# Kernel optimization log

Hardware: AMD Instinct MI355X
Metric: run time of the kernel (lower is better)

The kernel has to match this reference:

```python
import jax, jax.numpy as jnp
import numpy as np

B, S, HID = 1, 2048, 2048
H, KV, D = 32, 8, 64          # num_heads, num_kv_heads, head_dim
N_REP = H // KV               # GQA groups = 4
FF = 8192
EPS = 1e-5
ROPE_THETA = 10000.0


def _rope_tables(seq_len, dim, dtype=jnp.float32):
    inv_freq = 1.0 / (ROPE_THETA ** (jnp.arange(0, dim, 2, dtype=jnp.float32) / dim))
    t = jnp.arange(seq_len, dtype=jnp.float32)
    freqs = jnp.outer(t, inv_freq)                 # [S, D/2]
    emb = jnp.concatenate([freqs, freqs], axis=-1) # [S, D]
    return jnp.cos(emb).astype(dtype)[None], jnp.sin(emb).astype(dtype)[None]  # [1,S,D]


def setup_inputs() -> dict:
    key = jax.random.key(0)
    ks = jax.random.split(key, 10)
    s = 0.02
    cos, sin = _rope_tables(S, D)
    return {
        "hidden_states": jax.random.normal(ks[0], (B, S, HID), jnp.float32),
        "cos": cos, "sin": sin,
        "wq": jax.random.normal(ks[1], (HID, H * D), jnp.float32) * s,
        "wk": jax.random.normal(ks[2], (HID, KV * D), jnp.float32) * s,
        "wv": jax.random.normal(ks[3], (HID, KV * D), jnp.float32) * s,
        "wo": jax.random.normal(ks[4], (H * D, HID), jnp.float32) * s,
        "w_ln1": jnp.ones((HID,), jnp.float32),
        "w_ln2": jnp.ones((HID,), jnp.float32),
        "w_gate": jax.random.normal(ks[5], (HID, FF), jnp.float32) * s,
        "w_up": jax.random.normal(ks[6], (HID, FF), jnp.float32) * s,
        "w_down": jax.random.normal(ks[7], (FF, HID), jnp.float32) * s,
    }


def _rmsnorm(x, w):
    var = jnp.mean(jnp.square(x), axis=-1, keepdims=True)
    return x * jax.lax.rsqrt(var + EPS) * w


def _rotate_half(x):
    x1, x2 = jnp.split(x, 2, axis=-1)
    return jnp.concatenate([-x2, x1], axis=-1)


def _apply_rope(q, k, cos, sin):
    # q,k: [B,H,S,D]; cos,sin: [B,S,D] -> unsqueeze head dim
    c, s = cos[:, None], sin[:, None]
    return q * c + _rotate_half(q) * s, k * c + _rotate_half(k) * s


def reference(hidden_states, cos, sin, wq, wk, wv, wo, w_ln1, w_ln2, w_gate, w_up, w_down):
    residual = hidden_states
    x = _rmsnorm(hidden_states, w_ln1)

    q = (x @ wq).reshape(B, S, H, D).transpose(0, 2, 1, 3)    # [B,H,S,D]
    k = (x @ wk).reshape(B, S, KV, D).transpose(0, 2, 1, 3)   # [B,KV,S,D]
    v = (x @ wv).reshape(B, S, KV, D).transpose(0, 2, 1, 3)
    q, k = _apply_rope(q, k, cos, sin)

    # repeat_kv (interleaved) for GQA
    k = jnp.repeat(k, N_REP, axis=1)                           # [B,H,S,D]
    v = jnp.repeat(v, N_REP, axis=1)

    scale = 1.0 / np.sqrt(D)
    scores = jnp.einsum("bhqd,bhkd->bhqk", q, k) * scale       # [B,H,S,S]
    causal = jnp.tril(jnp.ones((S, S), bool))
    scores = jnp.where(causal, scores, jnp.finfo(scores.dtype).min)
    probs = jax.nn.softmax(scores, axis=-1)
    attn = jnp.einsum("bhqk,bhkd->bhqd", probs, v)             # [B,H,S,D]
    attn = attn.transpose(0, 2, 1, 3).reshape(B, S, H * D)
    attn = attn @ wo

    h = residual + attn
    residual = h
    y = _rmsnorm(h, w_ln2)
    mlp = (jax.nn.silu(y @ w_gate) * (y @ w_up)) @ w_down
    return residual + mlp
```

## Files before the change

### kernel.cpp

```cpp
#include <hip/hip_runtime.h>
#include <hip/hip_bf16.h>
#include <cstdint>

#define S_LEN 2048
#define HIDN  2048
#define NH    32
#define NKV   8
#define HD    64
#define FFN   8192
#define QKVN  3072
#define QKVLD 3072

typedef __attribute__((ext_vector_type(4)))  float f32x4;
typedef __attribute__((ext_vector_type(16))) float f32x16;
typedef __attribute__((ext_vector_type(8)))  short short8;
typedef __attribute__((ext_vector_type(4)))  short s16x4;

__device__ __forceinline__ short f2bf(float f) {
  union { float f; uint32_t u; } v; v.f = f;
  uint32_t r = v.u + 0x7FFFu + ((v.u >> 16) & 1u);
  return (short)(r >> 16);
}
__device__ __forceinline__ float bf2f(short s) {
  union { float f; uint32_t u; } v; v.u = ((uint32_t)(uint16_t)s) << 16;
  return v.f;
}
__device__ __forceinline__ unsigned packbf2(float lo, float hi) {
  return (unsigned)(uint16_t)f2bf(lo) | ((unsigned)(uint16_t)f2bf(hi) << 16);
}

#define GLOAD_LDS16(gp, lp) \
  __builtin_amdgcn_global_load_lds((const __attribute__((address_space(1))) void*)(gp), \
                                   (__attribute__((address_space(3))) void*)(lp), 16, 0, 0)

#define BARRIER()  asm volatile("s_barrier" ::: "memory")
#define LGKM0()    asm volatile("s_waitcnt lgkmcnt(0)" ::: "memory")
#define SCHED0()   __builtin_amdgcn_sched_barrier(0)
#define VMCNT(N)   asm volatile("s_waitcnt vmcnt(%0)" :: "n"(N) : "memory")

__global__ __launch_bounds__(256) void convT_kernel(const float* __restrict__ src,
    short* __restrict__ dst, int K, int N) {
  __shared__ float t[64][65];
  const int k0 = blockIdx.x * 64, n0 = blockIdx.y * 64;
  const int tr = threadIdx.x >> 4, tc = (threadIdx.x & 15) * 4;
  #pragma unroll
  for (int i = 0; i < 4; ++i) {
    float4 v = *(const float4*)(src + (size_t)(k0 + tr + i * 16) * N + n0 + tc);
    t[tr + i * 16][tc] = v.x; t[tr + i * 16][tc + 1] = v.y;
    t[tr + i * 16][tc + 2] = v.z; t[tr + i * 16][tc + 3] = v.w;
  }
  __syncthreads();
  const int dr = threadIdx.x >> 2, dc = (threadIdx.x & 3) * 16;
  short8 o0, o1;
  #pragma unroll
  for (int j = 0; j < 8; ++j) { o0[j] = f2bf(t[dc + j][dr]); o1[j] = f2bf(t[dc + 8 + j][dr]); }
  short* dp = dst + (size_t)(n0 + dr) * K + k0 + dc;
  *(short8*)dp = o0;
  *(short8*)(dp + 8) = o1;
}

__global__ __launch_bounds__(256) void rmsnorm_kernel(const float* __restrict__ X,
    const float* __restrict__ W, short* __restrict__ Y) {
  int row = blockIdx.x;
  const float4* x4 = (const float4*)(X + (size_t)row * HIDN);
  const float4* w4 = (const float4*)W;
  float4 v0 = x4[2 * threadIdx.x];
  float4 v1 = x4[2 * threadIdx.x + 1];
  float ss = v0.x*v0.x + v0.y*v0.y + v0.z*v0.z + v0.w*v0.w
           + v1.x*v1.x + v1.y*v1.y + v1.z*v1.z + v1.w*v1.w;
  #pragma unroll
  for (int off = 32; off > 0; off >>= 1) ss += __shfl_xor(ss, off, 64);
  __shared__ float red[4];
  if ((threadIdx.x & 63) == 0) red[threadIdx.x >> 6] = ss;
  __syncthreads();
  ss = red[0] + red[1] + red[2] + red[3];
  float rs = rsqrtf(ss * (1.0f / HIDN) + 1e-5f);
  float4 w0 = w4[2 * threadIdx.x], w1 = w4[2 * threadIdx.x + 1];
  short8 o;
  o[0] = f2bf(v0.x * rs * w0.x); o[1] = f2bf(v0.y * rs * w0.y);
  o[2] = f2bf(v0.z * rs * w0.z); o[3] = f2bf(v0.w * rs * w0.w);
  o[4] = f2bf(v1.x * rs * w1.x); o[5] = f2bf(v1.y * rs * w1.y);
  o[6] = f2bf(v1.z * rs * w1.z); o[7] = f2bf(v1.w * rs * w1.w);
  *(short8*)(Y + (size_t)row * HIDN + threadIdx.x * 8) = o;
}

template<int EPI, int BN>
__global__ __launch_bounds__(512, 1) void gemm8p(const short* __restrict__ A,
    const short* __restrict__ BT, void* __restrict__ Cp, const void* __restrict__ Xp,
    int N, int Kfull, int KC, int gy) {
  constexpr int NFN = BN / 64;
  constexpr int LB  = BN / 128;
  constexpr int VN  = 2 + 2 * LB;
  __shared__ __align__(16) short As[2][256 * 64];
  __shared__ __align__(16) short Bs[2][BN * 64];
  const int tid = threadIdx.x, lane = tid & 63, w = tid >> 6;
  const int wm2 = w >> 2;
  const int wn = (w & 3) * (BN / 4);
  const int l15 = lane & 15, lg = lane >> 4;
  const int cpx = gy >> 3;
  const int xcd = blockIdx.x & 7, cid = blockIdx.x >> 3;
  const int by = xcd * cpx + cid % cpx, bx = cid / cpx;
  const int brow = bx * 256, bcol = by * BN;
  const size_t kbase = (size_t)blockIdx.z * KC;
  const int r8 = lane >> 3, c8 = lane & 7;
  const int gblk = c8 ^ r8;
  const int nt = KC / 64;
  f32x4 acc[8][NFN] = {};
  short8 af[4], bf[2][NFN];

  auto STA = [&](int p, int kt, int h) {
    const size_t kc = kbase + (size_t)kt * 64 + gblk * 8;
    #pragma unroll
    for (int j = 0; j < 2; ++j) {
      const short* g = A + (size_t)(brow + h * 128 + j * 64 + w * 8 + r8) * Kfull + kc;
      GLOAD_LDS16(g, &As[p][(h * 128 + j * 64 + w * 8) * 64]);
    }
  };
  auto STB = [&](int p, int kt, int h) {
    const size_t kc = kbase + (size_t)kt * 64 + gblk * 8;
    #pragma unroll
    for (int j = 0; j < LB; ++j) {
      const short* g = BT + (size_t)(bcol + h * (BN / 2) + j * 64 + w * 8 + r8) * Kfull + kc;
      GLOAD_LDS16(g, &Bs[p][(h * (BN / 2) + j * 64 + w * 8) * 64]);
    }
  };
  auto LDA = [&](int p, int mh, int kk) {
    #pragma unroll
    for (int m = 0; m < 4; ++m) {
      const int row = mh * 128 + wm2 * 64 + m * 16 + l15;
      af[m] = *(const short8*)&As[p][row * 64 + (((kk * 4 + lg) ^ (row & 7)) * 8)];
    }
  };
  auto LDB = [&](int p, int kk) {
    #pragma unroll
    for (int n = 0; n < NFN; ++n) {
      const int row = wn + n * 16 + l15;
      bf[kk][n] = *(const short8*)&Bs[p][row * 64 + (((kk * 4 + lg) ^ (row & 7)) * 8)];
    }
  };

#define MMQ(MH, KK) \
  __builtin_amdgcn_s_setprio(1); \
  _Pragma("unroll") \
  for (int m = 0; m < 4; ++m) \
    _Pragma("unroll") \
    for (int n = 0; n < NFN; ++n) \
      acc[(MH) * 4 + m][n] = __builtin_amdgcn_mfma_f32_16x16x32_bf16(af[m], bf[KK][n], acc[(MH) * 4 + m][n], 0, 0, 0); \
  __builtin_amdgcn_s_setprio(0);

  STB(0, 0, 0); STB(0, 0, 1); STA(0, 0, 0); STA(0, 0, 1);
  STB(1, 1, 0); STB(1, 1, 1); STA(1, 1, 0);
  VMCNT(VN);
  BARRIER();

  for (int i = 0; i < nt / 2; ++i) {
    const int t = 2 * i;
    const bool li = (i == nt / 2 - 1);
    LDA(0, 0, 0); LDB(0, 0); LDB(0, 1);
    STA(1, t + 1, 1);
    BARRIER(); LGKM0(); SCHED0();
    MMQ(0, 0);
    BARRIER();
    LDA(0, 0, 1);
    if (!li) STB(0, t + 2, 0);
    BARRIER(); LGKM0(); SCHED0();
    MMQ(0, 1);
    BARRIER();
    LDA(0, 1, 0);
    if (!li) STB(0, t + 2, 1);
    BARRIER(); LGKM0(); SCHED0();
    MMQ(1, 0);
    BARRIER();
    LDA(0, 1, 1);
    if (!li) STA(0, t + 2, 0);
    BARRIER(); LGKM0(); SCHED0();
    MMQ(1, 1);
    if (li) { VMCNT(0); } else { VMCNT(VN); }
    BARRIER();
    LDA(1, 0, 0); LDB(1, 0); LDB(1, 1);
    if (!li) STA(0, t + 2, 1);
    BARRIER(); LGKM0(); SCHED0();
    MMQ(0, 0);
    BARRIER();
    LDA(1, 0, 1);
    if (!li) STB(1, t + 3, 0);
    BARRIER(); LGKM0(); SCHED0();
    MMQ(0, 1);
    BARRIER();
    LDA(1, 1, 0);
    if (!li) STB(1, t + 3, 1);
    BARRIER(); LGKM0(); SCHED0();
    MMQ(1, 0);
    BARRIER();
    LDA(1, 1, 1);
    if (!li) STA(1, t + 3, 0);
    BARRIER(); LGKM0(); SCHED0();
    MMQ(1, 1);
    if (!li) { VMCNT(VN); }
    BARRIER();
  }
#undef MMQ

  #pragma unroll
  for (int mf = 0; mf < 8; ++mf) {
    const int r0 = brow + (mf >> 2) * 128 + wm2 * 64 + (mf & 3) * 16 + lg * 4;
    #pragma unroll
    for (int nf = 0; nf < NFN; ++nf) {
      const int c = bcol + wn + nf * 16 + l15;
      #pragma unroll
      for (int i4 = 0; i4 < 4; ++i4) {
        const size_t idx = (size_t)(r0 + i4) * N + c;
        float v = acc[mf][nf][i4];
        if (EPI == 0) ((short*)Cp)[idx] = f2bf(v);
        if (EPI == 2) {
          float gf = bf2f(((const short*)Xp)[idx]);
          ((short*)Cp)[idx] = f2bf(gf / (1.f + __expf(-gf)) * v);
        }
        if (EPI == 3) ((float*)Cp)[(size_t)blockIdx.z * S_LEN * N + idx] = v;
      }
    }
  }
}

template<int EPI>
__global__ __launch_bounds__(256) void gemm_bt(const short* __restrict__ A,
    const short* __restrict__ BT, void* __restrict__ Cp, const void* __restrict__ Xp,
    int M, int N, int Kfull, int KC, int gx) {
  __shared__ __align__(16) short Ass[128 * 64];
  __shared__ __align__(16) short Bss[128 * 64];
  const int tid = threadIdx.x, lane = tid & 63, w = tid >> 6;
  const int wm = (w >> 1) * 64, wn = (w & 1) * 64;
  const int l15 = lane & 15, lg = lane >> 4;
  const int nwg = gridDim.x;
  const int qq = nwg >> 3, xcd = blockIdx.x & 7, off = blockIdx.x >> 3;
  const int wg = xcd * qq + off;
  const int brow = (wg % gx) * 128, bcol = (wg / gx) * 128;
  const size_t kbase = (size_t)blockIdx.y * KC;
  const int srow8 = lane >> 3;
  const int gblk  = (lane & 7) ^ (srow8 & 7);
  f32x4 acc[4][4] = {};

  for (int k0 = 0; k0 < KC; k0 += 64) {
    #pragma unroll
    for (int j = 0; j < 4; ++j) {
      const int rbase = w * 32 + j * 8;
      const int row = rbase + srow8;
      const short* ga = A + (size_t)(brow + row) * Kfull + kbase + k0 + gblk * 8;
      GLOAD_LDS16(ga, Ass + rbase * 64);
      const short* gb = BT + (size_t)(bcol + row) * Kfull + kbase + k0 + gblk * 8;
      GLOAD_LDS16(gb, Bss + rbase * 64);
    }
    __syncthreads();
    #pragma unroll
    for (int kk = 0; kk < 2; ++kk) {
      short8 af[4], bf[4];
      #pragma unroll
      for (int m = 0; m < 4; ++m) {
        const int row = wm + m * 16 + l15;
        af[m] = *(const short8*)&Ass[row * 64 + (((kk * 4 + lg) ^ (l15 & 7)) * 8)];
      }
      #pragma unroll
      for (int n = 0; n < 4; ++n) {
        const int row = wn + n * 16 + l15;
        bf[n] = *(const short8*)&Bss[row * 64 + (((kk * 4 + lg) ^ (l15 & 7)) * 8)];
      }
      #pragma unroll
      for (int m = 0; m < 4; ++m)
        #pragma unroll
        for (int n = 0; n < 4; ++n)
          acc[m][n] = __builtin_amdgcn_mfma_f32_16x16x32_bf16(af[m], bf[n], acc[m][n], 0, 0, 0);
    }
    __syncthreads();
  }

  const int r0 = brow + wm + lg * 4;
  const int c0 = bcol + wn + l15;
  #pragma unroll
  for (int m = 0; m < 4; ++m)
    #pragma unroll
    for (int n = 0; n < 4; ++n)
      #pragma unroll
      for (int i = 0; i < 4; ++i) {
        const size_t idx = (size_t)(r0 + m * 16 + i) * N + (c0 + n * 16);
        float v = acc[m][n][i];
        if (EPI == 0) ((short*)Cp)[idx] = f2bf(v);
        if (EPI == 1) ((float*)Cp)[idx] = v + ((const float*)Xp)[idx];
        if (EPI == 2) {
          float gf = bf2f(((const short*)Xp)[idx]);
          ((short*)Cp)[idx] = f2bf(gf / (1.f + __expf(-gf)) * v);
        }
        if (EPI == 3) ((float*)Cp)[(size_t)blockIdx.y * M * N + idx] = v;
      }
}

__global__ __launch_bounds__(256) void rope_kernel(short* __restrict__ qkv,
    const float* __restrict__ cosb, const float* __restrict__ sinb) {
  int idx = blockIdx.x * 256 + threadIdx.x;
  int d = idx & 31;
  int hh = (idx >> 5) % (NH + NKV);
  int s = idx / (32 * (NH + NKV));
  int col = (hh < NH) ? hh * HD : HIDN + (hh - NH) * HD;
  short* base = qkv + (size_t)s * QKVLD + col;
  float c  = cosb[s * HD + d];
  float sn = sinb[s * HD + d];
  float x1 = bf2f(base[d]), x2 = bf2f(base[d + 32]);
  base[d]      = f2bf(x1 * c - x2 * sn);
  base[d + 32] = f2bf(x2 * c + x1 * sn);
}

__global__ __launch_bounds__(256) void attn_kernel(const short* __restrict__ QKV,
    short* __restrict__ O) {
  __shared__ __align__(16) short Ks[64][72];
  __shared__ __align__(16) short VTs[64][72];
  const int bid = blockIdx.x;
  const int half = bid >> 8, idx = bid & 255;
  const int h = idx & 31;
  int qt = idx >> 5;
  qt = half ? (15 - qt) : qt;
  const int kvh = h >> 2;
  const int tid = threadIdx.x, lane = tid & 63, w = tid >> 6;
  const int l31 = lane & 31, hi = lane >> 5;
  const int qb = qt * 128 + w * 32;
  const int kcol = HIDN + kvh * HD;
  const int vcol = HIDN + NKV * HD + kvh * HD;

  short8 Qr[4];
  {
    const short* qp = QKV + (size_t)(qb + l31) * QKVLD + h * HD;
    #pragma unroll
    for (int dk = 0; dk < 4; ++dk) {
      short8 qv = *(const short8*)(qp + dk * 16 + hi * 8);
      #pragma unroll
      for (int e = 0; e < 8; ++e) Qr[dk][e] = f2bf(bf2f(qv[e]) * 0.125f);
    }
  }
  float m_ = -3e38f, l_ = 0.f;
  f32x16 o0 = {}, o1 = {};
  const int nt = 2 * qt + 2;
  const int krow = tid >> 2, kcb = (tid & 3) * 16;
  const int vk = tid & 31, vdb = (tid >> 5) * 8;

  for (int t = 0; t < nt; ++t) {
    const int kb = t * 64;
    __syncthreads();
    {
      const short* gk = QKV + (size_t)(kb + krow) * QKVLD + kcol + kcb;
      short8 a = *(const short8*)gk;
      short8 b = *(const short8*)(gk + 8);
      *(short8*)&Ks[krow][kcb] = a;
      *(short8*)&Ks[krow][kcb + 8] = b;
    }
    #pragma unroll
    for (int i = 0; i < 2; ++i) {
      const int k = i * 32 + vk;
      short8 v = *(const short8*)(QKV + (size_t)(kb + k) * QKVLD + vcol + vdb);
      #pragma unroll
      for (int j = 0; j < 8; ++j) VTs[vdb + j][k] = v[j];
    }
    __syncthreads();
    if (kb < qb + 32) {
      f32x16 s[2] = {};
      #pragma unroll
      for (int kt = 0; kt < 2; ++kt)
        #pragma unroll
        for (int dk = 0; dk < 4; ++dk) {
          short8 kf = *(const short8*)&Ks[kt * 32 + l31][dk * 16 + hi * 8];
          s[kt] = __builtin_amdgcn_mfma_f32_32x32x16_bf16(kf, Qr[dk], s[kt], 0, 0, 0);
        }
      if (kb + 63 > qb) {
        const int qg = qb + l31;
        #pragma unroll
        for (int kt = 0; kt < 2; ++kt)
          #pragma unroll
          for (int r = 0; r < 16; ++r) {
            const int kg = kb + kt * 32 + (r & 3) + 8 * (r >> 2) + 4 * hi;
            if (kg > qg) s[kt][r] = -1e30f;
          }
      }
      float pm = s[0][0];
      #pragma unroll
      for (int r = 1; r < 16; ++r) pm = fmaxf(pm, s[0][r]);
      #pragma unroll
      for (int r = 0; r < 16; ++r) pm = fmaxf(pm, s[1][r]);
      pm = fmaxf(pm, __shfl_xor(pm, 32));
      const float mn = fmaxf(m_, pm);
      const float al = __expf(m_ - mn);
      float rsum = 0.f;
      #pragma unroll
      for (int kt = 0; kt < 2; ++kt)
        #pragma unroll
        for (int r = 0; r < 16; ++r) { s[kt][r] = __expf(s[kt][r] - mn); rsum += s[kt][r]; }
      rsum += __shfl_xor(rsum, 32);
      l_ = l_ * al + rsum;
      m_ = mn;
      o0 *= al; o1 *= al;
      unsigned wd[2][8], rw[2][8];
      #pragma unroll
      for (int kt = 0; kt < 2; ++kt)
        #pragma unroll
        for (int i = 0; i < 8; ++i) {
          wd[kt][i] = packbf2(s[kt][2 * i], s[kt][2 * i + 1]);
          rw[kt][i] = (unsigned)__shfl_xor((int)wd[kt][i], 32);
        }
      #pragma unroll
      for (int kt = 0; kt < 2; ++kt) {
        union { unsigned u[4]; short8 s8; } pf0, pf1;
        if (hi) {
          pf0.u[0] = rw[kt][2]; pf0.u[1] = rw[kt][3]; pf0.u[2] = wd[kt][2]; pf0.u[3] = wd[kt][3];
          pf1.u[0] = rw[kt][6]; pf1.u[1] = rw[kt][7]; pf1.u[2] = wd[kt][6]; pf1.u[3] = wd[kt][7];
        } else {
          pf0.u[0] = wd[kt][0]; pf0.u[1] = wd[kt][1]; pf0.u[2] = rw[kt][0]; pf0.u[3] = rw[kt][1];
          pf1.u[0] = wd[kt][4]; pf1.u[1] = wd[kt][5]; pf1.u[2] = rw[kt][4]; pf1.u[3] = rw[kt][5];
        }
        #pragma unroll
        for (int ks = 0; ks < 2; ++ks) {
          const short8 pB = ks ? pf1.s8 : pf0.s8;
          short8 va = *(const short8*)&VTs[l31][kt * 32 + ks * 16 + hi * 8];
          o0 = __builtin_amdgcn_mfma_f32_32x32x16_bf16(va, pB, o0, 0, 0, 0);
          short8 vb = *(const short8*)&VTs[32 + l31][kt * 32 + ks * 16 + hi * 8];
          o1 = __builtin_amdgcn_mfma_f32_32x32x16_bf16(vb, pB, o1, 0, 0, 0);
        }
      }
    }
  }
  const float inv = 1.f / l_;
  short* op = O + (size_t)(qb + l31) * HIDN + h * HD;
  #pragma unroll
  for (int dt = 0; dt < 2; ++dt) {
    const f32x16& o = dt ? o1 : o0;
    #pragma unroll
    for (int g = 0; g < 4; ++g) {
      s16x4 st;
      st[0] = f2bf(o[g * 4 + 0] * inv);
      st[1] = f2bf(o[g * 4 + 1] * inv);
      st[2] = f2bf(o[g * 4 + 2] * inv);
      st[3] = f2bf(o[g * 4 + 3] * inv);
      *(s16x4*)(op + dt * 32 + g * 8 + hi * 4) = st;
    }
  }
}

__global__ __launch_bounds__(256) void reduce_kernel(float* __restrict__ out,
    const float* __restrict__ P) {
  const size_t n = (size_t)S_LEN * HIDN;
  size_t i = ((size_t)blockIdx.x * 256 + threadIdx.x) * 4;
  float4 o = *(float4*)(out + i);
  float4 a = *(const float4*)(P + i);
  float4 b = *(const float4*)(P + n + i);
  o.x += a.x + b.x; o.y += a.y + b.y; o.z += a.z + b.z; o.w += a.w + b.w;
  *(float4*)(out + i) = o;
}

extern "C" void kernel_launch(void* const* d_in, const int* in_sizes, int n_in,
                              void* d_out, int out_size, void* d_ws, size_t ws_size,
                              hipStream_t stream) {
  const float* hs   = (const float*)d_in[0];
  const float* cosb = (const float*)d_in[1];
  const float* sinb = (const float*)d_in[2];
  const float* wq   = (const float*)d_in[3];
  const float* wk   = (const float*)d_in[4];
  const float* wv   = (const float*)d_in[5];
  const float* wo   = (const float*)d_in[6];
  const float* wln1 = (const float*)d_in[7];
  const float* wln2 = (const float*)d_in[8];
  const float* wg   = (const float*)d_in[9];
  const float* wu   = (const float*)d_in[10];
  const float* wd   = (const float*)d_in[11];
  float* out = (float*)d_out;
  char* ws = (char*)d_ws;
  const size_t MB = 1024 * 1024;
  short* xn    = (short*)(ws);
  short* y     = (short*)(ws + 8 * MB);
  short* attnO = (short*)(ws + 16 * MB);
  short* qkv   = (short*)(ws + 24 * MB);
  short* g     = (short*)(ws + 37 * MB);
  short* Wbuf  = (short*)(ws + 69 * MB);
  float* P     = (float*)(ws);

  convT_kernel<<<dim3(32, 32), 256, 0, stream>>>(wq, Wbuf, HIDN, NH * HD);
  convT_kernel<<<dim3(32, 8),  256, 0, stream>>>(wk, Wbuf + (size_t)2048 * HIDN, HIDN, NKV * HD);
  convT_kernel<<<dim3(32, 8),  256, 0, stream>>>(wv, Wbuf + (size_t)2560 * HIDN, HIDN, NKV * HD);
  rmsnorm_kernel<<<S_LEN, 256, 0, stream>>>(hs, wln1, xn);
  gemm8p<0, 128><<<dim3(192, 1, 1), 512, 0, stream>>>(xn, Wbuf, qkv, nullptr, QKVN, HIDN, HIDN, 24);
  convT_kernel<<<dim3(32, 32), 256, 0, stream>>>(wo, Wbuf, NH * HD, HIDN);
  rope_kernel<<<(S_LEN * (NH + NKV) * 32) / 256, 256, 0, stream>>>(qkv, cosb, sinb);
  attn_kernel<<<NH * (S_LEN / 128), 256, 0, stream>>>(qkv, attnO);
  gemm_bt<1><<<dim3(16 * 16, 1), 256, 0, stream>>>(attnO, Wbuf, out, hs, S_LEN, HIDN, NH * HD, NH * HD, 16);
  rmsnorm_kernel<<<S_LEN, 256, 0, stream>>>(out, wln2, y);
  convT_kernel<<<dim3(32, 128), 256, 0, stream>>>(wg, Wbuf, HIDN, FFN);
  gemm8p<0, 256><<<dim3(256, 1, 1), 512, 0, stream>>>(y, Wbuf, g, nullptr, FFN, HIDN, HIDN, 32);
  convT_kernel<<<dim3(32, 128), 256, 0, stream>>>(wu, Wbuf, HIDN, FFN);
  gemm8p<2, 256><<<dim3(256, 1, 1), 512, 0, stream>>>(y, Wbuf, g, g, FFN, HIDN, HIDN, 32);
  convT_kernel<<<dim3(128, 32), 256, 0, stream>>>(wd, Wbuf, FFN, HIDN);
  gemm8p<3, 128><<<dim3(128, 1, 2), 512, 0, stream>>>(g, Wbuf, P, nullptr, HIDN, FFN, FFN / 2, 16);
  reduce_kernel<<<(S_LEN * HIDN) / 1024, 256, 0, stream>>>(out, P);
}
```

Before: 463.7 us.

## Prefetch attention K/V tiles into registers, relax GEMM waits, vectorize epilogue stores

The attention kernel now loads the next K/V tile into registers while the current tile is being computed, so global latency overlaps with the MFMA work. It also raises wave priority around the MFMA loops. In the big GEMM, the per-quarter lgkmcnt(0) waits and scheduling barriers are removed, leaving the compiler to insert waits. The epilogue pairs adjacent columns through a lane shuffle so even lanes store two values at once. The risk is extra register pressure in attention, and possible reordering hazards in the GEMM from dropping the explicit waits and sched barriers.

Result: slower. 639.5 us (+37.9%).

```diff
diff --git a/kernel.cpp b/kernel.cpp
--- a/kernel.cpp
+++ b/kernel.cpp
@@ -35,7 +35,6 @@
 
 #define BARRIER()  asm volatile("s_barrier" ::: "memory")
 #define LGKM0()    asm volatile("s_waitcnt lgkmcnt(0)" ::: "memory")
-#define SCHED0()   __builtin_amdgcn_sched_barrier(0)
 #define VMCNT(N)   asm volatile("s_waitcnt vmcnt(%0)" :: "n"(N) : "memory")
 
 __global__ __launch_bounds__(256) void convT_kernel(const float* __restrict__ src,
@@ -158,65 +157,81 @@
     const bool li = (i == nt / 2 - 1);
     LDA(0, 0, 0); LDB(0, 0); LDB(0, 1);
     STA(1, t + 1, 1);
-    BARRIER(); LGKM0(); SCHED0();
+    BARRIER();
     MMQ(0, 0);
+    LGKM0();
     BARRIER();
     LDA(0, 0, 1);
     if (!li) STB(0, t + 2, 0);
-    BARRIER(); LGKM0(); SCHED0();
+    BARRIER();
     MMQ(0, 1);
     BARRIER();
     LDA(0, 1, 0);
     if (!li) STB(0, t + 2, 1);
-    BARRIER(); LGKM0(); SCHED0();
+    BARRIER();
     MMQ(1, 0);
     BARRIER();
     LDA(0, 1, 1);
     if (!li) STA(0, t + 2, 0);
-    BARRIER(); LGKM0(); SCHED0();
+    BARRIER();
     MMQ(1, 1);
     if (li) { VMCNT(0); } else { VMCNT(VN); }
     BARRIER();
     LDA(1, 0, 0); LDB(1, 0); LDB(1, 1);
     if (!li) STA(0, t + 2, 1);
-    BARRIER(); LGKM0(); SCHED0();
+    BARRIER();
     MMQ(0, 0);
+    LGKM0();
     BARRIER();
     LDA(1, 0, 1);
     if (!li) STB(1, t + 3, 0);
-    BARRIER(); LGKM0(); SCHED0();
+    BARRIER();
     MMQ(0, 1);
     BARRIER();
     LDA(1, 1, 0);
     if (!li) STB(1, t + 3, 1);
-    BARRIER(); LGKM0(); SCHED0();
+    BARRIER();
     MMQ(1, 0);
     BARRIER();
     LDA(1, 1, 1);
     if (!li) STA(1, t + 3, 0);
-    BARRIER(); LGKM0(); SCHED0();
+    BARRIER();
     MMQ(1, 1);
     if (!li) { VMCNT(VN); }
     BARRIER();
   }
 #undef MMQ
 
+  const bool evn = (l15 & 1) == 0;
   #pragma unroll
   for (int mf = 0; mf < 8; ++mf) {
     const int r0 = brow + (mf >> 2) * 128 + wm2 * 64 + (mf & 3) * 16 + lg * 4;
     #pragma unroll
     for (int nf = 0; nf < NFN; ++nf) {
-      const int c = bcol + wn + nf * 16 + l15;
+      const int cp = bcol + wn + nf * 16 + (l15 & ~1);
       #pragma unroll
       for (int i4 = 0; i4 < 4; ++i4) {
-        const size_t idx = (size_t)(r0 + i4) * N + c;
+        const size_t idx = (size_t)(r0 + i4) * N + cp;
         float v = acc[mf][nf][i4];
-        if (EPI == 0) ((short*)Cp)[idx] = f2bf(v);
+        float vo = __shfl_xor(v, 1);
+        if (EPI == 0) {
+          if (evn) *(unsigned*)((short*)Cp + idx) = packbf2(v, vo);
+        }
         if (EPI == 2) {
-          float gf = bf2f(((const short*)Xp)[idx]);
-          ((short*)Cp)[idx] = f2bf(gf / (1.f + __expf(-gf)) * v);
-        }
-        if (EPI == 3) ((float*)Cp)[(size_t)blockIdx.z * S_LEN * N + idx] = v;
+          unsigned xw = evn ? *(const unsigned*)((const short*)Xp + idx) : 0u;
+          if (evn) {
+            float xl = bf2f((short)(xw & 0xFFFF)), xh = bf2f((short)(xw >> 16));
+            float w0 = xl / (1.f + __expf(-xl)) * v;
+            float w1 = xh / (1.f + __expf(-xh)) * vo;
+            *(unsigned*)((short*)Cp + idx) = packbf2(w0, w1);
+          }
+        }
+        if (EPI == 3) {
+          if (evn) {
+            float2 st; st.x = v; st.y = vo;
+            *(float2*)((float*)Cp + (size_t)blockIdx.z * S_LEN * N + idx) = st;
+          }
+        }
       }
     }
   }
@@ -340,26 +355,35 @@
   const int krow = tid >> 2, kcb = (tid & 3) * 16;
   const int vk = tid & 31, vdb = (tid >> 5) * 8;
 
+  short8 kr0, kr1, vr0, vr1;
+  {
+    const short* gk = QKV + (size_t)krow * QKVLD + kcol + kcb;
+    kr0 = *(const short8*)gk; kr1 = *(const short8*)(gk + 8);
+    vr0 = *(const short8*)(QKV + (size_t)vk * QKVLD + vcol + vdb);
+    vr1 = *(const short8*)(QKV + (size_t)(32 + vk) * QKVLD + vcol + vdb);
+  }
+
   for (int t = 0; t < nt; ++t) {
     const int kb = t * 64;
-    __syncthreads();
-    {
-      const short* gk = QKV + (size_t)(kb + krow) * QKVLD + kcol + kcb;
-      short8 a = *(const short8*)gk;
-      short8 b = *(const short8*)(gk + 8);
-      *(short8*)&Ks[krow][kcb] = a;
-      *(short8*)&Ks[krow][kcb + 8] = b;
-    }
-    #pragma unroll
-    for (int i = 0; i < 2; ++i) {
-      const int k = i * 32 + vk;
-      short8 v = *(const short8*)(QKV + (size_t)(kb + k) * QKVLD + vcol + vdb);
-      #pragma unroll
-      for (int j = 0; j < 8; ++j) VTs[vdb + j][k] = v[j];
-    }
-    __syncthreads();
+    BARRIER();
+    *(short8*)&Ks[krow][kcb] = kr0;
+    *(short8*)&Ks[krow][kcb + 8] = kr1;
+    #pragma unroll
+    for (int j = 0; j < 8; ++j) VTs[vdb + j][vk] = vr0[j];
+    #pragma unroll
+    for (int j = 0; j < 8; ++j) VTs[vdb + j][32 + vk] = vr1[j];
+    LGKM0();
+    BARRIER();
+    if (t + 1 < nt) {
+      const int kb2 = kb + 64;
+      const short* gk = QKV + (size_t)(kb2 + krow) * QKVLD + kcol + kcb;
+      kr0 = *(const short8*)gk; kr1 = *(const short8*)(gk + 8);
+      vr0 = *(const short8*)(QKV + (size_t)(kb2 + vk) * QKVLD + vcol + vdb);
+      vr1 = *(const short8*)(QKV + (size_t)(kb2 + 32 + vk) * QKVLD + vcol + vdb);
+    }
     if (kb < qb + 32) {
       f32x16 s[2] = {};
+      __builtin_amdgcn_s_setprio(1);
       #pragma unroll
       for (int kt = 0; kt < 2; ++kt)
         #pragma unroll
@@ -367,6 +391,7 @@
           short8 kf = *(const short8*)&Ks[kt * 32 + l31][dk * 16 + hi * 8];
           s[kt] = __builtin_amdgcn_mfma_f32_32x32x16_bf16(kf, Qr[dk], s[kt], 0, 0, 0);
         }
+      __builtin_amdgcn_s_setprio(0);
       if (kb + 63 > qb) {
         const int qg = qb + l31;
         #pragma unroll
@@ -412,6 +437,7 @@
           pf0.u[0] = wd[kt][0]; pf0.u[1] = wd[kt][1]; pf0.u[2] = rw[kt][0]; pf0.u[3] = rw[kt][1];
           pf1.u[0] = wd[kt][4]; pf1.u[1] = wd[kt][5]; pf1.u[2] = rw[kt][4]; pf1.u[3] = rw[kt][5];
         }
+        __builtin_amdgcn_s_setprio(1);
         #pragma unroll
         for (int ks = 0; ks < 2; ++ks) {
           const short8 pB = ks ? pf1.s8 : pf0.s8;
@@ -420,6 +446,7 @@
           short8 vb = *(const short8*)&VTs[32 + l31][kt * 32 + ks * 16 + hi * 8];
           o1 = __builtin_amdgcn_mfma_f32_32x32x16_bf16(vb, pB, o1, 0, 0, 0);
         }
+        __builtin_amdgcn_s_setprio(0);
       }
     }
   }
```
